# Kernel tuning notes

Hardware: AMD Instinct MI355X
Metric: run time of the kernel (lower is better)

The kernel has to match this reference:

```python
import jax, jax.numpy as jnp
import numpy as np

ALPHA = 0.2          # LeakyReLU slope
COUNTER_COEFF = 0.5  # config.counter_coeff
N = 50000
E = 500000
NFEATS = 256
NHIDS = 256
NHEADS = 8
DH = NHIDS // NHEADS


def _gat_multihead(x_src, x_dst, src, dst, W, b, a_s, a_d, a_b, n_dst):
    """Multi-head GAT: gather-linear-leakyrelu edge attention, segment softmax,
    softmax-weighted scatter sum.  W:[H,F,D] b:[H,D] a_s,a_d:[H,D] a_b:[H].
    Returns [n_dst, H*D] (heads concatenated, as torch.cat over heads)."""
    Wh_s = jnp.einsum('nf,hfd->nhd', x_src, W) + b  # [Ns,H,D]
    Wh_d = jnp.einsum('nf,hfd->nhd', x_dst, W) + b  # [Nd,H,D]
    # a([Wh_src;Wh_dst]) decomposes into src and dst halves of the weight
    es = jnp.einsum('nhd,hd->nh', Wh_s, a_s)
    ed = jnp.einsum('nhd,hd->nh', Wh_d, a_d)
    e = jax.nn.leaky_relu(es[src] + ed[dst] + a_b, ALPHA)  # [E,H]
    # per-destination (mailbox) softmax, numerically stable
    emax = jax.ops.segment_max(e, dst, num_segments=n_dst)
    emax = jnp.where(jnp.isfinite(emax), emax, 0.0)
    ex = jnp.exp(e - emax[dst])
    denom = jax.ops.segment_sum(ex, dst, num_segments=n_dst)
    att = ex / denom[dst]                          # every edge's dst has >=1 edge
    msg = att[:, :, None] * Wh_s[src]              # [E,H,D]
    out = jax.ops.segment_sum(msg, dst, num_segments=n_dst)  # [n_dst,H,D]
    return out.reshape(n_dst, -1)


def _gru_cell(x, h, W_ih, W_hh, b_ih, b_hh):
    gi = x @ W_ih.T + b_ih
    gh = h @ W_hh.T + b_hh
    i_r, i_z, i_n = jnp.split(gi, 3, axis=1)
    h_r, h_z, h_n = jnp.split(gh, 3, axis=1)
    r = jax.nn.sigmoid(i_r + h_r)
    z = jax.nn.sigmoid(i_z + h_z)
    n = jnp.tanh(i_n + r * h_n)
    return (1.0 - z) * n + z * h


def setup_inputs() -> dict:
    key = jax.random.key(0)
    ks = jax.random.split(key, 20)
    xavier = lambda k, shape, fin, fout: jax.random.uniform(
        k, shape, jnp.float32, -1.0, 1.0) * (1.414 * np.sqrt(6.0 / (fin + fout)))
    inp = {}
    inp['h'] = jax.random.normal(ks[0], (N, NFEATS), jnp.float32)
    inp['hp_counter'] = jax.random.normal(ks[1], (N, NHIDS), jnp.float32)
    inp['hp_support'] = jax.random.normal(ks[2], (N, NHIDS), jnp.float32)
    inp['hp_dst'] = jax.random.normal(ks[3], (N, NHIDS), jnp.float32)
    # intra-turn GAT weights (per head)
    inp['W_gat'] = xavier(ks[4], (NHEADS, NFEATS, DH), NFEATS, DH)
    inp['b_gat'] = jnp.zeros((NHEADS, DH), jnp.float32)
    inp['as_gat'] = xavier(ks[5], (NHEADS, DH), 2 * DH, 1)
    inp['ad_gat'] = xavier(ks[6], (NHEADS, DH), 2 * DH, 1)
    inp['ab_gat'] = jnp.zeros((NHEADS,), jnp.float32)
    # cross-turn GAT weights (shared for counter & support: same self.xgat)
    inp['W_x'] = xavier(ks[7], (NHEADS, NHIDS, DH), NHIDS, DH)
    inp['b_x'] = jnp.zeros((NHEADS, DH), jnp.float32)
    inp['as_x'] = xavier(ks[8], (NHEADS, DH), 2 * DH, 1)
    inp['ad_x'] = xavier(ks[9], (NHEADS, DH), 2 * DH, 1)
    inp['ab_x'] = jnp.zeros((NHEADS,), jnp.float32)
    # GRUCell(nhids, nhids)
    s = 1.0 / np.sqrt(NHIDS)
    inp['W_ih'] = jax.random.uniform(ks[10], (3 * NHIDS, NHIDS), jnp.float32, -s, s)
    inp['W_hh'] = jax.random.uniform(ks[11], (3 * NHIDS, NHIDS), jnp.float32, -s, s)
    inp['b_ih'] = jax.random.uniform(ks[12], (3 * NHIDS,), jnp.float32, -s, s)
    inp['b_hh'] = jax.random.uniform(ks[13], (3 * NHIDS,), jnp.float32, -s, s)
    # edge lists
    inp['edge_src'] = jax.random.randint(ks[14], (E,), 0, N, jnp.int32)
    inp['edge_dst'] = jax.random.randint(ks[15], (E,), 0, N, jnp.int32)
    inp['edge_c_src'] = jax.random.randint(ks[16], (E,), 0, N, jnp.int32)
    inp['edge_c_dst'] = jax.random.randint(ks[17], (E,), 0, N, jnp.int32)
    inp['edge_s_src'] = jax.random.randint(ks[18], (E,), 0, N, jnp.int32)
    inp['edge_s_dst'] = jax.random.randint(ks[19], (E,), 0, N, jnp.int32)
    return inp


def reference(h, hp_counter, hp_support, hp_dst,
              W_gat, b_gat, as_gat, ad_gat, ab_gat,
              W_x, b_x, as_x, ad_x, ab_x,
              W_ih, W_hh, b_ih, b_hh,
              edge_src, edge_dst, edge_c_src, edge_c_dst,
              edge_s_src, edge_s_dst):
    # x = self.gat(g, t): intra-turn multi-head GAT on raw features h
    x = _gat_multihead(h, h, edge_src, edge_dst,
                       W_gat, b_gat, as_gat, ad_gat, ab_gat, N)
    # h_c = self.xgat(g, t-1, 'counter'): directed GAT, prev-turn -> current
    h_c = _gat_multihead(hp_counter, hp_dst, edge_c_src, edge_c_dst,
                         W_x, b_x, as_x, ad_x, ab_x, N)
    # h_s = self.xgat(g, t-2, 'support') (same weights)
    h_s = _gat_multihead(hp_support, hp_dst, edge_s_src, edge_s_dst,
                         W_x, b_x, as_x, ad_x, ab_x, N)
    hmix = COUNTER_COEFF * h_c + (1.0 - COUNTER_COEFF) * h_s
    hprime = _gru_cell(x, hmix, W_ih, W_hh, b_ih, b_hh)
    return hprime
```

## Files before the change

kernel.cpp:

```cpp
#include <hip/hip_runtime.h>
#include <math.h>

#define ALPHA 0.2f
#define LOG2E 1.44269504088896f

constexpr int FEATS = 256;
constexpr int HEADS = 8;

typedef unsigned short u16;
typedef __attribute__((ext_vector_type(8))) short bf16x8;
typedef __attribute__((ext_vector_type(4))) float f32x4;

__device__ __forceinline__ u16 f2b(float f) {
    unsigned u = __float_as_uint(f);
    u += 0x7FFF + ((u >> 16) & 1);
    return (u16)(u >> 16);
}
__device__ __forceinline__ float b2f(u16 x) {
    return __uint_as_float(((unsigned)x) << 16);
}
__device__ __forceinline__ unsigned pk2(float lo, float hi) {
    return __builtin_amdgcn_perm(__float_as_uint(hi), __float_as_uint(lo), 0x07060302u);
}
__device__ __forceinline__ void gload16(const void* g, void* l) {
    __builtin_amdgcn_global_load_lds(
        (const __attribute__((address_space(1))) unsigned int*)g,
        (__attribute__((address_space(3))) unsigned int*)l, 16, 0, 0);
}

__global__ __launch_bounds__(256) void proj4_kernel(
    const float* __restrict__ A0, const float* __restrict__ A1,
    const float* __restrict__ A2, const float* __restrict__ A3,
    const u16* __restrict__ Bg, const u16* __restrict__ Bx,
    const float* __restrict__ bg, const float* __restrict__ bx,
    u16* __restrict__ C0, u16* __restrict__ C1,
    u16* __restrict__ C2, u16* __restrict__ C3,
    int M, int NB) {
    __shared__ char As_raw[32768];
    __shared__ char Bs_raw[16384];
    const int tid = threadIdx.x;
    const int lane = tid & 63;
    const int wid = tid >> 6;
    const int wr = wid >> 1, wc = wid & 1;
    const int seg = blockIdx.y / NB;
    const int bm = (blockIdx.y % NB) * 128;
    const int bn = blockIdx.x * 128;
    const float* A = (seg == 0) ? A0 : (seg == 1) ? A1 : (seg == 2) ? A2 : A3;
    const u16* B = (seg == 0) ? Bg : Bx;
    const float* bias = (seg == 0) ? bg : bx;
    u16* C = (seg == 0) ? C0 : (seg == 1) ? C1 : (seg == 2) ? C2 : C3;

    f32x4 acc[4][4];
#pragma unroll
    for (int m = 0; m < 4; ++m)
#pragma unroll
        for (int n = 0; n < 4; ++n) acc[m][n] = (f32x4)0.f;

    for (int kb = 0; kb < 4; ++kb) {
        const int k0g = kb * 64;
#pragma unroll
        for (int i = 0; i < 8; ++i) {
            int s = i * 256 + tid;
            int row = s >> 4, c16 = s & 15;
            int c32 = c16 >> 1, half = c16 & 1;
            int gr = min(bm + row, M - 1);
            int gcol = k0g + ((c32 ^ (row & 7)) * 8 + half * 4);
            gload16(A + (size_t)gr * 256 + gcol, As_raw + s * 16);
        }
#pragma unroll
        for (int i = 0; i < 4; ++i) {
            int s = i * 256 + tid;
            int row = s >> 3, c16 = s & 7;
            int gcol = k0g + (c16 ^ (row & 7)) * 8;
            gload16(B + (size_t)(bn + row) * 256 + gcol, Bs_raw + s * 16);
        }
        __syncthreads();
#pragma unroll
        for (int kk = 0; kk < 2; ++kk) {
            const int ko = kk * 32 + (lane >> 4) * 8;
            const int kc = ko >> 3;
            bf16x8 af[4], bfr[4];
#pragma unroll
            for (int m = 0; m < 4; ++m) {
                int row = wr * 64 + m * 16 + (lane & 15);
                int byte = row * 256 + ((kc ^ (row & 7)) << 5);
                f32x4 lo = *(const f32x4*)(As_raw + byte);
                f32x4 hi = *(const f32x4*)(As_raw + byte + 16);
                union { unsigned u[4]; bf16x8 v; } cv;
                cv.u[0] = pk2(lo.x, lo.y); cv.u[1] = pk2(lo.z, lo.w);
                cv.u[2] = pk2(hi.x, hi.y); cv.u[3] = pk2(hi.z, hi.w);
                af[m] = cv.v;
            }
#pragma unroll
            for (int n = 0; n < 4; ++n) {
                int row = wc * 64 + n * 16 + (lane & 15);
                int byte = row * 128 + ((kc ^ (row & 7)) << 4);
                bfr[n] = *(const bf16x8*)(Bs_raw + byte);
            }
#pragma unroll
            for (int m = 0; m < 4; ++m)
#pragma unroll
                for (int n = 0; n < 4; ++n)
                    acc[m][n] = __builtin_amdgcn_mfma_f32_16x16x32_bf16(
                        af[m], bfr[n], acc[m][n], 0, 0, 0);
        }
        __syncthreads();
    }
#pragma unroll
    for (int m = 0; m < 4; ++m) {
#pragma unroll
        for (int j = 0; j < 4; ++j) {
            int gr = bm + wr * 64 + m * 16 + (lane >> 4) * 4 + j;
            if (gr < M) {
#pragma unroll
                for (int n = 0; n < 4; ++n) {
                    int gc = bn + wc * 64 + n * 16 + (lane & 15);
                    C[(size_t)gr * 256 + gc] = f2b(acc[m][n][j] + bias[gc]);
                }
            }
        }
    }
}

__global__ void prep_kernel(const float* __restrict__ W_gat, const float* __restrict__ W_x,
                            const float* __restrict__ W_ih, const float* __restrict__ W_hh,
                            u16* __restrict__ Bgat, u16* __restrict__ Bx,
                            u16* __restrict__ Bihr, u16* __restrict__ Bhhr) {
    int i = blockIdx.x * 256 + threadIdx.x;
    if (i < 131072) {
        int j = i & 65535;
        int n = j >> 8, f = j & 255;
        int h2 = n >> 5, d = n & 31;
        const float* W = (i < 65536) ? W_gat : W_x;
        u16* Bt = (i < 65536) ? Bgat : Bx;
        Bt[j] = f2b(W[(h2 * 256 + f) * 32 + d]);
    } else {
        int x = i - 131072;
        int lin = (x < 196608) ? x : x - 196608;
        int c = lin >> 8, k = lin & 255;
        int q = c / 48, rr = c - q * 48;
        int g = rr >> 4, jl = rr & 15;
        int orig = (g * 256 + q * 16 + jl) * 256 + k;
        if (x < 196608) Bihr[lin] = f2b(W_ih[orig]);
        else            Bhhr[lin] = f2b(W_hh[orig]);
    }
}

__global__ void esed_all_kernel(
    const u16* __restrict__ Wh1, const u16* __restrict__ WhC,
    const u16* __restrict__ WhD, const u16* __restrict__ WhS3,
    const float* __restrict__ as_g, const float* __restrict__ ad_g,
    const float* __restrict__ as_x, const float* __restrict__ ad_x,
    float* __restrict__ es1, float* __restrict__ ed1,
    float* __restrict__ esC, float* __restrict__ edD,
    float* __restrict__ esS, int n) {
    int idx = blockIdx.x * blockDim.x + threadIdx.x;
    if (idx >= n * 8) return;
    int node = idx >> 3, hh = idx & 7;
    float s1 = 0.f, d1 = 0.f, sC = 0.f, dD = 0.f, sS = 0.f;
#pragma unroll
    for (int i = 0; i < 8; ++i) {
        const float4 wsg = *(const float4*)(as_g + hh * 32 + i * 4);
        const float4 wdg = *(const float4*)(ad_g + hh * 32 + i * 4);
        const float4 wsx = *(const float4*)(as_x + hh * 32 + i * 4);
        const float4 wdx = *(const float4*)(ad_x + hh * 32 + i * 4);
        ushort4 v1 = *(const ushort4*)(Wh1 + (size_t)node * FEATS + hh * 32 + i * 4);
        ushort4 vC = *(const ushort4*)(WhC + (size_t)node * FEATS + hh * 32 + i * 4);
        ushort4 vD = *(const ushort4*)(WhD + (size_t)node * FEATS + hh * 32 + i * 4);
        ushort4 vS = *(const ushort4*)(WhS3 + (size_t)node * FEATS + hh * 32 + i * 4);
        s1 += b2f(v1.x) * wsg.x + b2f(v1.y) * wsg.y + b2f(v1.z) * wsg.z + b2f(v1.w) * wsg.w;
        d1 += b2f(v1.x) * wdg.x + b2f(v1.y) * wdg.y + b2f(v1.z) * wdg.z + b2f(v1.w) * wdg.w;
        sC += b2f(vC.x) * wsx.x + b2f(vC.y) * wsx.y + b2f(vC.z) * wsx.z + b2f(vC.w) * wsx.w;
        dD += b2f(vD.x) * wdx.x + b2f(vD.y) * wdx.y + b2f(vD.z) * wdx.z + b2f(vD.w) * wdx.w;
        sS += b2f(vS.x) * wsx.x + b2f(vS.y) * wsx.y + b2f(vS.z) * wsx.z + b2f(vS.w) * wsx.w;
    }
    es1[idx] = s1 * LOG2E; ed1[idx] = d1 * LOG2E;
    esC[idx] = sC * LOG2E; edD[idx] = dD * LOG2E;
    esS[idx] = sS * LOG2E;
}

__global__ void count3_kernel(const int* __restrict__ d0, const int* __restrict__ d1,
                              const int* __restrict__ d2, int* __restrict__ cnt,
                              int E, int N) {
    int i = blockIdx.x * blockDim.x + threadIdx.x;
    if (i >= 3 * E) return;
    if (i < E) atomicAdd(&cnt[d0[i]], 1);
    else if (i < 2 * E) atomicAdd(&cnt[N + d1[i - E]], 1);
    else atomicAdd(&cnt[2 * N + d2[i - 2 * E]], 1);
}
__global__ void scan1_kernel(const int* __restrict__ cnt, int* __restrict__ off,
                             int* __restrict__ blksum, int n) {
    __shared__ int tmp[256];
    int t = threadIdx.x;
    int base = blockIdx.x * 1024 + t * 4;
    int v[4];
#pragma unroll
    for (int k = 0; k < 4; ++k) v[k] = (base + k < n) ? cnt[base + k] : 0;
    int s = v[0] + v[1] + v[2] + v[3];
    tmp[t] = s;
    __syncthreads();
    for (int st = 1; st < 256; st <<= 1) {
        int add = (t >= st) ? tmp[t - st] : 0;
        __syncthreads();
        tmp[t] += add;
        __syncthreads();
    }
    int ex = tmp[t] - s;
#pragma unroll
    for (int k = 0; k < 4; ++k) {
        if (base + k < n) off[base + k] = ex;
        ex += v[k];
    }
    if (t == 255) blksum[blockIdx.x] = tmp[255];
}
__global__ void scan2_kernel(int* __restrict__ blksum, int nb) {
    __shared__ int tmp[256];
    int t = threadIdx.x;
    int v = (t < nb) ? blksum[t] : 0;
    tmp[t] = v;
    __syncthreads();
    for (int s = 1; s < 256; s <<= 1) {
        int add = (t >= s) ? tmp[t - s] : 0;
        __syncthreads();
        tmp[t] += add;
        __syncthreads();
    }
    if (t < nb) blksum[t] = tmp[t] - v;
}
__global__ void scan3_kernel(int* __restrict__ off, int* __restrict__ cur,
                             const int* __restrict__ blksum, int n) {
    int i = blockIdx.x * blockDim.x + threadIdx.x;
    if (i < n) {
        int v = off[i] + blksum[i >> 10];
        off[i] = v;
        cur[i] = v;
    }
}
__global__ void fill3_kernel(const int* __restrict__ s0, const int* __restrict__ d0,
                             const int* __restrict__ s1, const int* __restrict__ d1,
                             const int* __restrict__ s2, const int* __restrict__ d2,
                             int* __restrict__ cur, int* __restrict__ srcs, int E, int N) {
    int i = blockIdx.x * blockDim.x + threadIdx.x;
    if (i >= 3 * E) return;
    int s, slot;
    if (i < E) { s = s0[i]; slot = d0[i]; }
    else if (i < 2 * E) { s = s1[i - E]; slot = N + d1[i - E]; }
    else { s = s2[i - 2 * E]; slot = 2 * N + d2[i - 2 * E]; }
    int p = atomicAdd(&cur[slot], 1);
    srcs[p] = s;
}

__device__ __forceinline__ void run_seg(
    const int* __restrict__ srcs, int start, int deg,
    const float* __restrict__ es, const u16* __restrict__ Wh,
    float edv, int o, int hh,
    float& psum, float4& a) {
    float m = -1e30f;
    psum = 0.f;
    a = make_float4(0.f, 0.f, 0.f, 0.f);
    if (deg <= 0) return;
    int sP = srcs[start];
    int sN = (deg > 1) ? srcs[start + 1] : sP;
    float rawP = es[sP * 8 + hh];
    ushort4 wP = *(const ushort4*)(Wh + (size_t)sP * FEATS + o);
    for (int j = 0; j < deg; ++j) {
        int sNN = (j + 2 < deg) ? srcs[start + j + 2] : sN;
        float rawN = es[sN * 8 + hh];
        ushort4 wN = *(const ushort4*)(Wh + (size_t)sN * FEATS + o);
        float e = rawP + edv;
        e = e > 0.f ? e : ALPHA * e;
        float mn = fmaxf(m, e);
        float rr = exp2f(m - mn);
        float pe = exp2f(e - mn);
        psum = psum * rr + pe;
        a.x = a.x * rr + pe * b2f(wP.x);
        a.y = a.y * rr + pe * b2f(wP.y);
        a.z = a.z * rr + pe * b2f(wP.z);
        a.w = a.w * rr + pe * b2f(wP.w);
        m = mn;
        rawP = rawN; wP = wN; sN = sNN;
    }
}

__global__ __launch_bounds__(256) void gather_all_kernel(
    const int* __restrict__ off, const int* __restrict__ cnt,
    const int* __restrict__ srcs,
    const float* __restrict__ es1, const float* __restrict__ ed1,
    const float* __restrict__ esC, const float* __restrict__ edD,
    const float* __restrict__ esS,
    const float* __restrict__ ab_g, const float* __restrict__ ab_x,
    const u16* __restrict__ Wh1, const u16* __restrict__ WhC,
    const u16* __restrict__ WhS3,
    u16* __restrict__ xb, u16* __restrict__ hmixb, int N) {
    int gwid = (blockIdx.x * blockDim.x + threadIdx.x) >> 6;
    if (gwid >= 2 * N) return;
    int lane = threadIdx.x & 63;
    int o = lane * 4, hh = lane >> 3;
    if (gwid < N) {
        int node = gwid;
        float edv = ed1[node * 8 + hh] + ab_g[hh] * LOG2E;
        float psum; float4 a;
        run_seg(srcs, off[node], cnt[node], es1, Wh1, edv, o, hh, psum, a);
        float sc = (cnt[node] > 0) ? (1.0f / psum) : 0.f;
        ushort4 r;
        r.x = f2b(a.x * sc); r.y = f2b(a.y * sc);
        r.z = f2b(a.z * sc); r.w = f2b(a.w * sc);
        *(ushort4*)(xb + (size_t)node * FEATS + o) = r;
    } else {
        int node = gwid - N;
        float edv = edD[node * 8 + hh] + ab_x[hh] * LOG2E;
        float psum2; float4 a2;
        run_seg(srcs, off[N + node], cnt[N + node], esC, WhC, edv, o, hh, psum2, a2);
        float sc2 = (cnt[N + node] > 0) ? (0.5f / psum2) : 0.f;
        float psum3; float4 a3;
        run_seg(srcs, off[2 * N + node], cnt[2 * N + node], esS, WhS3, edv, o, hh, psum3, a3);
        float sc3 = (cnt[2 * N + node] > 0) ? (0.5f / psum3) : 0.f;
        ushort4 r;
        r.x = f2b(a2.x * sc2 + a3.x * sc3);
        r.y = f2b(a2.y * sc2 + a3.y * sc3);
        r.z = f2b(a2.z * sc2 + a3.z * sc3);
        r.w = f2b(a2.w * sc2 + a3.w * sc3);
        *(ushort4*)(hmixb + (size_t)node * FEATS + o) = r;
    }
}

__device__ __forceinline__ void gemm_pass_gru(
    const u16* __restrict__ A, const u16* __restrict__ B,
    int bm, int bt, int M, char* As, char* Bs,
    int tid, int lane, int wr, int wc, f32x4 (&acc)[4][3]) {
    for (int kb = 0; kb < 4; ++kb) {
        const int k0g = kb * 64;
#pragma unroll
        for (int i = 0; i < 4; ++i) {
            int s = i * 256 + tid;
            int row = s >> 3, c16 = s & 7;
            int gr = min(bm + row, M - 1);
            int gcol = k0g + (c16 ^ (row & 7)) * 8;
            gload16(A + (size_t)gr * 256 + gcol, As + s * 16);
        }
#pragma unroll
        for (int i = 0; i < 3; ++i) {
            int s = i * 256 + tid;
            int row = s >> 3, c16 = s & 7;
            int gcol = k0g + (c16 ^ (row & 7)) * 8;
            gload16(B + (size_t)(bt * 96 + row) * 256 + gcol, Bs + s * 16);
        }
        __syncthreads();
#pragma unroll
        for (int kk = 0; kk < 2; ++kk) {
            const int ko = kk * 32 + (lane >> 4) * 8;
            const int kc = ko >> 3;
            bf16x8 af[4], bfr[3];
#pragma unroll
            for (int m = 0; m < 4; ++m) {
                int row = wr * 64 + m * 16 + (lane & 15);
                af[m] = *(const bf16x8*)(As + row * 128 + ((kc ^ (row & 7)) << 4));
            }
#pragma unroll
            for (int n = 0; n < 3; ++n) {
                int row = wc * 48 + n * 16 + (lane & 15);
                bfr[n] = *(const bf16x8*)(Bs + row * 128 + ((kc ^ (row & 7)) << 4));
            }
#pragma unroll
            for (int m = 0; m < 4; ++m)
#pragma unroll
                for (int n = 0; n < 3; ++n)
                    acc[m][n] = __builtin_amdgcn_mfma_f32_16x16x32_bf16(
                        af[m], bfr[n], acc[m][n], 0, 0, 0);
        }
        __syncthreads();
    }
}

__global__ __launch_bounds__(256) void gru_fused_kernel(
    const u16* __restrict__ xb, const u16* __restrict__ hmixb,
    const u16* __restrict__ Bihr, const u16* __restrict__ Bhhr,
    const float* __restrict__ b_ih, const float* __restrict__ b_hh,
    float* __restrict__ out, int M) {
    __shared__ char As[16384];
    __shared__ char Bs[12288];
    const int tid = threadIdx.x;
    const int lane = tid & 63;
    const int wid = tid >> 6;
    const int wr = wid >> 1, wc = wid & 1;
    const int bt = blockIdx.x;
    const int bm = blockIdx.y * 128;

    f32x4 agi[4][3], agh[4][3];
#pragma unroll
    for (int m = 0; m < 4; ++m)
#pragma unroll
        for (int n = 0; n < 3; ++n) { agi[m][n] = (f32x4)0.f; agh[m][n] = (f32x4)0.f; }

    gemm_pass_gru(xb, Bihr, bm, bt, M, As, Bs, tid, lane, wr, wc, agi);
    gemm_pass_gru(hmixb, Bhhr, bm, bt, M, As, Bs, tid, lane, wr, wc, agh);

    const int j = (bt * 2 + wc) * 16 + (lane & 15);
    const float bir = b_ih[j], biz = b_ih[256 + j], bin = b_ih[512 + j];
    const float bhr = b_hh[j], bhz = b_hh[256 + j], bhn = b_hh[512 + j];
#pragma unroll
    for (int m = 0; m < 4; ++m) {
#pragma unroll
        for (int jj = 0; jj < 4; ++jj) {
            int row = bm + wr * 64 + m * 16 + (lane >> 4) * 4 + jj;
            if (row < M) {
                float gr_ = agi[m][0][jj] + bir + agh[m][0][jj] + bhr;
                float gz_ = agi[m][1][jj] + biz + agh[m][1][jj] + bhz;
                float rr = 1.f / (1.f + exp2f(-gr_ * LOG2E));
                float zz = 1.f / (1.f + exp2f(-gz_ * LOG2E));
                float nn = tanhf(agi[m][2][jj] + bin + rr * (agh[m][2][jj] + bhn));
                float hm = b2f(hmixb[(size_t)row * 256 + j]);
                out[(size_t)row * 256 + j] = (1.f - zz) * nn + zz * hm;
            }
        }
    }
}

extern "C" void kernel_launch(void* const* d_in, const int* in_sizes, int n_in,
                              void* d_out, int out_size, void* d_ws, size_t ws_size,
                              hipStream_t stream) {
    const float* h        = (const float*)d_in[0];
    const float* hp_cnt   = (const float*)d_in[1];
    const float* hp_sup   = (const float*)d_in[2];
    const float* hp_dst   = (const float*)d_in[3];
    const float* W_gat    = (const float*)d_in[4];
    const float* b_gat    = (const float*)d_in[5];
    const float* as_gat   = (const float*)d_in[6];
    const float* ad_gat   = (const float*)d_in[7];
    const float* ab_gat   = (const float*)d_in[8];
    const float* W_x      = (const float*)d_in[9];
    const float* b_x      = (const float*)d_in[10];
    const float* as_x     = (const float*)d_in[11];
    const float* ad_x     = (const float*)d_in[12];
    const float* ab_x     = (const float*)d_in[13];
    const float* W_ih     = (const float*)d_in[14];
    const float* W_hh     = (const float*)d_in[15];
    const float* b_ih     = (const float*)d_in[16];
    const float* b_hh     = (const float*)d_in[17];
    const int* e_src      = (const int*)d_in[18];
    const int* e_dst      = (const int*)d_in[19];
    const int* ec_src     = (const int*)d_in[20];
    const int* ec_dst     = (const int*)d_in[21];
    const int* es_src     = (const int*)d_in[22];
    const int* es_dst     = (const int*)d_in[23];

    const int N = in_sizes[0] / FEATS;
    const int E = in_sizes[18];
    const int N8 = N * HEADS;
    const int N3 = 3 * N;
    const int NBLK3 = (N3 + 1023) / 1024;
    const int NB128 = (N + 127) / 128;

    char* ws = (char*)d_ws;
    size_t p = 0;
    u16* Wh1   = (u16*)(ws + p); p += (size_t)N * FEATS * 2;
    u16* WhC   = (u16*)(ws + p); p += (size_t)N * FEATS * 2;
    u16* WhD   = (u16*)(ws + p); p += (size_t)N * FEATS * 2;
    u16* WhS3  = (u16*)(ws + p); p += (size_t)N * FEATS * 2;
    u16* xb    = (u16*)(ws + p); p += (size_t)N * FEATS * 2;
    u16* hmixb = (u16*)(ws + p); p += (size_t)N * FEATS * 2;
    float* es1 = (float*)(ws + p); p += (size_t)N8 * 4;
    float* ed1 = (float*)(ws + p); p += (size_t)N8 * 4;
    float* esC = (float*)(ws + p); p += (size_t)N8 * 4;
    float* edD = (float*)(ws + p); p += (size_t)N8 * 4;
    float* esS = (float*)(ws + p); p += (size_t)N8 * 4;
    int* cnt3  = (int*)(ws + p); p += (size_t)N3 * 4;
    int* off3  = (int*)(ws + p); p += (size_t)N3 * 4;
    int* cur3  = (int*)(ws + p); p += (size_t)N3 * 4;
    int* blks  = (int*)(ws + p); p += 1024;
    int* srcs3 = (int*)(ws + p); p += (size_t)3 * E * 4;
    u16* Bgat  = (u16*)(ws + p); p += 65536 * 2;
    u16* Bx    = (u16*)(ws + p); p += 65536 * 2;
    u16* Bihr  = (u16*)(ws + p); p += 196608 * 2;
    u16* Bhhr  = (u16*)(ws + p); p += 196608 * 2;

    const dim3 blk(256);
    const int gN8 = (N8 + 255) / 256;
    const int g3E = (3 * E + 255) / 256;

    prep_kernel<<<2048, blk, 0, stream>>>(W_gat, W_x, W_ih, W_hh, Bgat, Bx, Bihr, Bhhr);
    hipMemsetAsync(cnt3, 0, (size_t)N3 * 4, stream);
    count3_kernel<<<g3E, blk, 0, stream>>>(e_dst, ec_dst, es_dst, cnt3, E, N);
    scan1_kernel<<<NBLK3, blk, 0, stream>>>(cnt3, off3, blks, N3);
    scan2_kernel<<<1, blk, 0, stream>>>(blks, NBLK3);
    scan3_kernel<<<(N3 + 255) / 256, blk, 0, stream>>>(off3, cur3, blks, N3);
    fill3_kernel<<<g3E, blk, 0, stream>>>(e_src, e_dst, ec_src, ec_dst, es_src, es_dst,
                                          cur3, srcs3, E, N);

    proj4_kernel<<<dim3(2, 4 * NB128), blk, 0, stream>>>(
        h, hp_cnt, hp_dst, hp_sup, Bgat, Bx, b_gat, b_x,
        Wh1, WhC, WhD, WhS3, N, NB128);

    esed_all_kernel<<<gN8, blk, 0, stream>>>(Wh1, WhC, WhD, WhS3,
                                             as_gat, ad_gat, as_x, ad_x,
                                             es1, ed1, esC, edD, esS, N);

    gather_all_kernel<<<(2 * N * 64 + 255) / 256, blk, 0, stream>>>(
        off3, cnt3, srcs3, es1, ed1, esC, edD, esS, ab_gat, ab_x,
        Wh1, WhC, WhS3, xb, hmixb, N);

    gru_fused_kernel<<<dim3(8, NB128), blk, 0, stream>>>(
        xb, hmixb, Bihr, Bhhr, b_ih, b_hh, (float*)d_out, N);
}
```

Before: 581.9 us.

## Fuse attention logits into projection GEMM, drop online-softmax max, widen GRU tiles

The per-node attention logits (es/ed) are now computed in the projection GEMM epilogue using 16-lane shuffle reductions, which removes the separate esed kernel and its re-read of four bf16 projection matrices. The gather loop stops tracking a running max and just accumulates exp2 of the logits, saving the rescale multiplies per edge, at the risk of overflow if logits get large. The GRU kernel now takes 192 columns of B per block (grid x goes from 8 to 4) and merges the r/z accumulation of both passes into one set of accumulators. This halves A-tile reloads but uses more registers and LDS.

```diff
diff --git a/kernel.cpp b/kernel.cpp
--- a/kernel.cpp
+++ b/kernel.cpp
@@ -26,6 +26,11 @@
     __builtin_amdgcn_global_load_lds(
         (const __attribute__((address_space(1))) unsigned int*)g,
         (__attribute__((address_space(3))) unsigned int*)l, 16, 0, 0);
+}
+__device__ __forceinline__ float rsum16(float v) {
+    v += __shfl_xor(v, 1); v += __shfl_xor(v, 2);
+    v += __shfl_xor(v, 4); v += __shfl_xor(v, 8);
+    return v;
 }
 
 __global__ __launch_bounds__(256) void proj4_kernel(
@@ -35,6 +40,11 @@
     const float* __restrict__ bg, const float* __restrict__ bx,
     u16* __restrict__ C0, u16* __restrict__ C1,
     u16* __restrict__ C2, u16* __restrict__ C3,
+    const float* __restrict__ as_g, const float* __restrict__ ad_g,
+    const float* __restrict__ as_x, const float* __restrict__ ad_x,
+    float* __restrict__ es1, float* __restrict__ ed1,
+    float* __restrict__ esC, float* __restrict__ edD,
+    float* __restrict__ esS,
     int M, int NB) {
     __shared__ char As_raw[32768];
     __shared__ char Bs_raw[16384];
@@ -49,6 +59,10 @@
     const u16* B = (seg == 0) ? Bg : Bx;
     const float* bias = (seg == 0) ? bg : bx;
     u16* C = (seg == 0) ? C0 : (seg == 1) ? C1 : (seg == 2) ? C2 : C3;
+    const float* asP = (seg == 0) ? as_g : (seg == 2) ? nullptr : as_x;
+    const float* adP = (seg == 0) ? ad_g : (seg == 2) ? ad_x : nullptr;
+    float* esP = (seg == 0) ? es1 : (seg == 1) ? esC : (seg == 3) ? esS : nullptr;
+    float* edP = (seg == 0) ? ed1 : (seg == 2) ? edD : nullptr;
 
     f32x4 acc[4][4];
 #pragma unroll
@@ -106,16 +120,41 @@
         }
         __syncthreads();
     }
+    const int l15 = lane & 15;
+    const int hb = (bn >> 5) + wc * 2;
+    float cS[4], cD[4];
+#pragma unroll
+    for (int n = 0; n < 4; ++n) {
+        int hn = hb + (n >> 1);
+        int ix = (n & 1) * 16 + l15;
+        cS[n] = asP ? asP[hn * 32 + ix] : 0.f;
+        cD[n] = adP ? adP[hn * 32 + ix] : 0.f;
+    }
 #pragma unroll
     for (int m = 0; m < 4; ++m) {
 #pragma unroll
         for (int j = 0; j < 4; ++j) {
             int gr = bm + wr * 64 + m * 16 + (lane >> 4) * 4 + j;
+            float tmp[4];
+#pragma unroll
+            for (int n = 0; n < 4; ++n)
+                tmp[n] = acc[m][n][j] + bias[bn + wc * 64 + n * 16 + l15];
             if (gr < M) {
 #pragma unroll
-                for (int n = 0; n < 4; ++n) {
-                    int gc = bn + wc * 64 + n * 16 + (lane & 15);
-                    C[(size_t)gr * 256 + gc] = f2b(acc[m][n][j] + bias[gc]);
+                for (int n = 0; n < 4; ++n)
+                    C[(size_t)gr * 256 + bn + wc * 64 + n * 16 + l15] = f2b(tmp[n]);
+            }
+#pragma unroll
+            for (int g = 0; g < 2; ++g) {
+                if (esP) {
+                    float ps = cS[2 * g] * tmp[2 * g] + cS[2 * g + 1] * tmp[2 * g + 1];
+                    ps = rsum16(ps);
+                    if (l15 == 0 && gr < M) esP[(size_t)gr * 8 + hb + g] = ps * LOG2E;
+                }
+                if (edP) {
+                    float pd = cD[2 * g] * tmp[2 * g] + cD[2 * g + 1] * tmp[2 * g + 1];
+                    pd = rsum16(pd);
+                    if (l15 == 0 && gr < M) edP[(size_t)gr * 8 + hb + g] = pd * LOG2E;
                 }
             }
         }
@@ -146,39 +185,6 @@
     }
 }
 
-__global__ void esed_all_kernel(
-    const u16* __restrict__ Wh1, const u16* __restrict__ WhC,
-    const u16* __restrict__ WhD, const u16* __restrict__ WhS3,
-    const float* __restrict__ as_g, const float* __restrict__ ad_g,
-    const float* __restrict__ as_x, const float* __restrict__ ad_x,
-    float* __restrict__ es1, float* __restrict__ ed1,
-    float* __restrict__ esC, float* __restrict__ edD,
-    float* __restrict__ esS, int n) {
-    int idx = blockIdx.x * blockDim.x + threadIdx.x;
-    if (idx >= n * 8) return;
-    int node = idx >> 3, hh = idx & 7;
-    float s1 = 0.f, d1 = 0.f, sC = 0.f, dD = 0.f, sS = 0.f;
-#pragma unroll
-    for (int i = 0; i < 8; ++i) {
-        const float4 wsg = *(const float4*)(as_g + hh * 32 + i * 4);
-        const float4 wdg = *(const float4*)(ad_g + hh * 32 + i * 4);
-        const float4 wsx = *(const float4*)(as_x + hh * 32 + i * 4);
-        const float4 wdx = *(const float4*)(ad_x + hh * 32 + i * 4);
-        ushort4 v1 = *(const ushort4*)(Wh1 + (size_t)node * FEATS + hh * 32 + i * 4);
-        ushort4 vC = *(const ushort4*)(WhC + (size_t)node * FEATS + hh * 32 + i * 4);
-        ushort4 vD = *(const ushort4*)(WhD + (size_t)node * FEATS + hh * 32 + i * 4);
-        ushort4 vS = *(const ushort4*)(WhS3 + (size_t)node * FEATS + hh * 32 + i * 4);
-        s1 += b2f(v1.x) * wsg.x + b2f(v1.y) * wsg.y + b2f(v1.z) * wsg.z + b2f(v1.w) * wsg.w;
-        d1 += b2f(v1.x) * wdg.x + b2f(v1.y) * wdg.y + b2f(v1.z) * wdg.z + b2f(v1.w) * wdg.w;
-        sC += b2f(vC.x) * wsx.x + b2f(vC.y) * wsx.y + b2f(vC.z) * wsx.z + b2f(vC.w) * wsx.w;
-        dD += b2f(vD.x) * wdx.x + b2f(vD.y) * wdx.y + b2f(vD.z) * wdx.z + b2f(vD.w) * wdx.w;
-        sS += b2f(vS.x) * wsx.x + b2f(vS.y) * wsx.y + b2f(vS.z) * wsx.z + b2f(vS.w) * wsx.w;
-    }
-    es1[idx] = s1 * LOG2E; ed1[idx] = d1 * LOG2E;
-    esC[idx] = sC * LOG2E; edD[idx] = dD * LOG2E;
-    esS[idx] = sS * LOG2E;
-}
-
 __global__ void count3_kernel(const int* __restrict__ d0, const int* __restrict__ d1,
                               const int* __restrict__ d2, int* __restrict__ cnt,
                               int E, int N) {
@@ -255,7 +261,6 @@
     const float* __restrict__ es, const u16* __restrict__ Wh,
     float edv, int o, int hh,
     float& psum, float4& a) {
-    float m = -1e30f;
     psum = 0.f;
     a = make_float4(0.f, 0.f, 0.f, 0.f);
     if (deg <= 0) return;
@@ -269,15 +274,12 @@
         ushort4 wN = *(const ushort4*)(Wh + (size_t)sN * FEATS + o);
         float e = rawP + edv;
         e = e > 0.f ? e : ALPHA * e;
-        float mn = fmaxf(m, e);
-        float rr = exp2f(m - mn);
-        float pe = exp2f(e - mn);
-        psum = psum * rr + pe;
-        a.x = a.x * rr + pe * b2f(wP.x);
-        a.y = a.y * rr + pe * b2f(wP.y);
-        a.z = a.z * rr + pe * b2f(wP.z);
-        a.w = a.w * rr + pe * b2f(wP.w);
-        m = mn;
+        float pe = exp2f(e);
+        psum += pe;
+        a.x += pe * b2f(wP.x);
+        a.y += pe * b2f(wP.y);
+        a.z += pe * b2f(wP.z);
+        a.w += pe * b2f(wP.w);
         rawP = rawN; wP = wN; sN = sNN;
     }
 }
@@ -324,93 +326,108 @@
     }
 }
 
-__device__ __forceinline__ void gemm_pass_gru(
-    const u16* __restrict__ A, const u16* __restrict__ B,
-    int bm, int bt, int M, char* As, char* Bs,
-    int tid, int lane, int wr, int wc, f32x4 (&acc)[4][3]) {
-    for (int kb = 0; kb < 4; ++kb) {
-        const int k0g = kb * 64;
-#pragma unroll
-        for (int i = 0; i < 4; ++i) {
-            int s = i * 256 + tid;
-            int row = s >> 3, c16 = s & 7;
-            int gr = min(bm + row, M - 1);
-            int gcol = k0g + (c16 ^ (row & 7)) * 8;
-            gload16(A + (size_t)gr * 256 + gcol, As + s * 16);
-        }
-#pragma unroll
-        for (int i = 0; i < 3; ++i) {
-            int s = i * 256 + tid;
-            int row = s >> 3, c16 = s & 7;
-            int gcol = k0g + (c16 ^ (row & 7)) * 8;
-            gload16(B + (size_t)(bt * 96 + row) * 256 + gcol, Bs + s * 16);
-        }
-        __syncthreads();
-#pragma unroll
-        for (int kk = 0; kk < 2; ++kk) {
-            const int ko = kk * 32 + (lane >> 4) * 8;
-            const int kc = ko >> 3;
-            bf16x8 af[4], bfr[3];
-#pragma unroll
-            for (int m = 0; m < 4; ++m) {
-                int row = wr * 64 + m * 16 + (lane & 15);
-                af[m] = *(const bf16x8*)(As + row * 128 + ((kc ^ (row & 7)) << 4));
-            }
-#pragma unroll
-            for (int n = 0; n < 3; ++n) {
-                int row = wc * 48 + n * 16 + (lane & 15);
-                bfr[n] = *(const bf16x8*)(Bs + row * 128 + ((kc ^ (row & 7)) << 4));
-            }
-#pragma unroll
-            for (int m = 0; m < 4; ++m)
-#pragma unroll
-                for (int n = 0; n < 3; ++n)
-                    acc[m][n] = __builtin_amdgcn_mfma_f32_16x16x32_bf16(
-                        af[m], bfr[n], acc[m][n], 0, 0, 0);
-        }
-        __syncthreads();
-    }
-}
-
 __global__ __launch_bounds__(256) void gru_fused_kernel(
     const u16* __restrict__ xb, const u16* __restrict__ hmixb,
     const u16* __restrict__ Bihr, const u16* __restrict__ Bhhr,
     const float* __restrict__ b_ih, const float* __restrict__ b_hh,
     float* __restrict__ out, int M) {
     __shared__ char As[16384];
-    __shared__ char Bs[12288];
+    __shared__ char Bs[24576];
     const int tid = threadIdx.x;
     const int lane = tid & 63;
     const int wid = tid >> 6;
     const int wr = wid >> 1, wc = wid & 1;
     const int bt = blockIdx.x;
     const int bm = blockIdx.y * 128;
-
-    f32x4 agi[4][3], agh[4][3];
-#pragma unroll
-    for (int m = 0; m < 4; ++m)
-#pragma unroll
-        for (int n = 0; n < 3; ++n) { agi[m][n] = (f32x4)0.f; agh[m][n] = (f32x4)0.f; }
-
-    gemm_pass_gru(xb, Bihr, bm, bt, M, As, Bs, tid, lane, wr, wc, agi);
-    gemm_pass_gru(hmixb, Bhhr, bm, bt, M, As, Bs, tid, lane, wr, wc, agh);
-
-    const int j = (bt * 2 + wc) * 16 + (lane & 15);
-    const float bir = b_ih[j], biz = b_ih[256 + j], bin = b_ih[512 + j];
-    const float bhr = b_hh[j], bhz = b_hh[256 + j], bhn = b_hh[512 + j];
+    const int l15 = lane & 15;
+
+    f32x4 acc[4][6], acc2[4][2];
+#pragma unroll
+    for (int m = 0; m < 4; ++m) {
+#pragma unroll
+        for (int n = 0; n < 6; ++n) acc[m][n] = (f32x4)0.f;
+        acc2[m][0] = (f32x4)0.f; acc2[m][1] = (f32x4)0.f;
+    }
+
+#pragma unroll
+    for (int pass = 0; pass < 2; ++pass) {
+        const u16* A = pass ? hmixb : xb;
+        const u16* B = pass ? Bhhr : Bihr;
+        for (int kb = 0; kb < 4; ++kb) {
+            const int k0g = kb * 64;
+#pragma unroll
+            for (int i = 0; i < 4; ++i) {
+                int s = i * 256 + tid;
+                int row = s >> 3, c16 = s & 7;
+                int gr = min(bm + row, M - 1);
+                int gcol = k0g + (c16 ^ (row & 7)) * 8;
+                gload16(A + (size_t)gr * 256 + gcol, As + s * 16);
+            }
+#pragma unroll
+            for (int i = 0; i < 6; ++i) {
+                int s = i * 256 + tid;
+                int row = s >> 3, c16 = s & 7;
+                int gcol = k0g + (c16 ^ (row & 7)) * 8;
+                gload16(B + (size_t)(bt * 192 + row) * 256 + gcol, Bs + s * 16);
+            }
+            __syncthreads();
+#pragma unroll
+            for (int kk = 0; kk < 2; ++kk) {
+                const int ko = kk * 32 + (lane >> 4) * 8;
+                const int kc = ko >> 3;
+                bf16x8 af[4], bfr[6];
+#pragma unroll
+                for (int m = 0; m < 4; ++m) {
+                    int row = wr * 64 + m * 16 + l15;
+                    af[m] = *(const bf16x8*)(As + row * 128 + ((kc ^ (row & 7)) << 4));
+                }
+#pragma unroll
+                for (int n = 0; n < 6; ++n) {
+                    int row = wc * 96 + (n / 3) * 48 + (n % 3) * 16 + l15;
+                    bfr[n] = *(const bf16x8*)(Bs + row * 128 + ((kc ^ (row & 7)) << 4));
+                }
+#pragma unroll
+                for (int m = 0; m < 4; ++m) {
+#pragma unroll
+                    for (int n = 0; n < 6; ++n) {
+                        if (pass == 1 && (n % 3) == 2)
+                            acc2[m][n / 3] = __builtin_amdgcn_mfma_f32_16x16x32_bf16(
+                                af[m], bfr[n], acc2[m][n / 3], 0, 0, 0);
+                        else
+                            acc[m][n] = __builtin_amdgcn_mfma_f32_16x16x32_bf16(
+                                af[m], bfr[n], acc[m][n], 0, 0, 0);
+                    }
+                }
+            }
+            __syncthreads();
+        }
+    }
+    float bir[2], biz[2], bin[2], bhr[2], bhz[2], bhn[2];
+    int jj2[2];
+#pragma unroll
+    for (int n3 = 0; n3 < 2; ++n3) {
+        int j = (bt * 4 + wc * 2 + n3) * 16 + l15;
+        jj2[n3] = j;
+        bir[n3] = b_ih[j]; biz[n3] = b_ih[256 + j]; bin[n3] = b_ih[512 + j];
+        bhr[n3] = b_hh[j]; bhz[n3] = b_hh[256 + j]; bhn[n3] = b_hh[512 + j];
+    }
 #pragma unroll
     for (int m = 0; m < 4; ++m) {
 #pragma unroll
         for (int jj = 0; jj < 4; ++jj) {
             int row = bm + wr * 64 + m * 16 + (lane >> 4) * 4 + jj;
             if (row < M) {
-                float gr_ = agi[m][0][jj] + bir + agh[m][0][jj] + bhr;
-                float gz_ = agi[m][1][jj] + biz + agh[m][1][jj] + bhz;
-                float rr = 1.f / (1.f + exp2f(-gr_ * LOG2E));
-                float zz = 1.f / (1.f + exp2f(-gz_ * LOG2E));
-                float nn = tanhf(agi[m][2][jj] + bin + rr * (agh[m][2][jj] + bhn));
-                float hm = b2f(hmixb[(size_t)row * 256 + j]);
-                out[(size_t)row * 256 + j] = (1.f - zz) * nn + zz * hm;
+#pragma unroll
+                for (int n3 = 0; n3 < 2; ++n3) {
+                    float gr_ = acc[m][n3 * 3 + 0][jj] + bir[n3] + bhr[n3];
+                    float gz_ = acc[m][n3 * 3 + 1][jj] + biz[n3] + bhz[n3];
+                    float rr = 1.f / (1.f + exp2f(-gr_ * LOG2E));
+                    float zz = 1.f / (1.f + exp2f(-gz_ * LOG2E));
+                    float nn = tanhf(acc[m][n3 * 3 + 2][jj] + bin[n3] +
+                                     rr * (acc2[m][n3][jj] + bhn[n3]));
+                    float hm = b2f(hmixb[(size_t)row * 256 + jj2[n3]]);
+                    out[(size_t)row * 256 + jj2[n3]] = (1.f - zz) * nn + zz * hm;
+                }
             }
         }
     }
@@ -475,7 +492,6 @@
     u16* Bhhr  = (u16*)(ws + p); p += 196608 * 2;
 
     const dim3 blk(256);
-    const int gN8 = (N8 + 255) / 256;
     const int g3E = (3 * E + 255) / 256;
 
     prep_kernel<<<2048, blk, 0, stream>>>(W_gat, W_x, W_ih, W_hh, Bgat, Bx, Bihr, Bhhr);
@@ -489,16 +505,14 @@
 
     proj4_kernel<<<dim3(2, 4 * NB128), blk, 0, stream>>>(
         h, hp_cnt, hp_dst, hp_sup, Bgat, Bx, b_gat, b_x,
-        Wh1, WhC, WhD, WhS3, N, NB128);
-
-    esed_all_kernel<<<gN8, blk, 0, stream>>>(Wh1, WhC, WhD, WhS3,
-                                             as_gat, ad_gat, as_x, ad_x,
-                                             es1, ed1, esC, edD, esS, N);
+        Wh1, WhC, WhD, WhS3,
+        as_gat, ad_gat, as_x, ad_x,
+        es1, ed1, esC, edD, esS, N, NB128);
 
     gather_all_kernel<<<(2 * N * 64 + 255) / 256, blk, 0, stream>>>(
         off3, cnt3, srcs3, es1, ed1, esC, edD, esS, ab_gat, ab_x,
         Wh1, WhC, WhS3, xb, hmixb, N);
 
-    gru_fused_kernel<<<dim3(8, NB128), blk, 0, stream>>>(
+    gru_fused_kernel<<<dim3(4, NB128), blk, 0, stream>>>(
         xb, hmixb, Bihr, Bhhr, b_ih, b_hh, (float*)d_out, N);
 }
```

Result: slower. 621.3 us (+6.8%).
